# Performance work log

Hardware: AMD Instinct MI355X
Metric: run time of the kernel (lower is better)

The kernel has to match this reference:

```python
import jax, jax.numpy as jnp
import numpy as np

N = 1048576   # collocation points
D_IN = 2      # PDE spatial dim
H = 256       # mlp_x hidden
R0 = R1 = R2 = 64  # Tucker ranks (mlp_quad_last_shape)
NQ0 = NQ1 = 1024   # quadrature points per axis (quad_concat)
HQ = 128      # mlp_quad hidden
HC = 128      # core_mlp hidden
C_IN = 64     # core_init feature dim


def _mlp(x, W1, b1, W2, b2):
    # 2-layer MLP with tanh, standing in for the torch nn.Sequential MLPs
    return jnp.tanh(x @ W1 + b1) @ W2 + b2


def _r_func(quad_x, eq_param):
    # quadrature weight per point, shape (n_i, 1)
    return jnp.sin(jnp.pi * eq_param[0] * quad_x)


def setup_inputs() -> dict:
    key = jax.random.key(0)
    ks = jax.random.split(key, 16)

    def rn(k, shape, fan_in):
        return jax.random.normal(k, shape, dtype=jnp.float32) / np.float32(np.sqrt(fan_in))

    return {
        "input": jax.random.normal(ks[0], (N, D_IN), dtype=jnp.float32),
        "eq_param": jnp.ones((1,), jnp.float32),
        "quad_x0": jax.random.uniform(ks[1], (NQ0, 1), dtype=jnp.float32),
        "quad_x1": jax.random.uniform(ks[2], (NQ1, 1), dtype=jnp.float32),
        "core_init": jax.random.normal(ks[3], (1, C_IN), dtype=jnp.float32),
        # mlp_x: D_IN -> H -> R0
        "Wx1": rn(ks[4], (D_IN, H), D_IN), "bx1": jnp.zeros((H,), jnp.float32),
        "Wx2": rn(ks[5], (H, R0), H), "bx2": jnp.zeros((R0,), jnp.float32),
        # mlp_quad[0]: 1 -> HQ -> R1
        "Wq01": rn(ks[6], (1, HQ), 1), "bq01": jnp.zeros((HQ,), jnp.float32),
        "Wq02": rn(ks[7], (HQ, R1), HQ), "bq02": jnp.zeros((R1,), jnp.float32),
        # mlp_quad[1]: 1 -> HQ -> R2
        "Wq11": rn(ks[8], (1, HQ), 1), "bq11": jnp.zeros((HQ,), jnp.float32),
        "Wq12": rn(ks[9], (HQ, R2), HQ), "bq12": jnp.zeros((R2,), jnp.float32),
        # core_mlp: C_IN -> HC -> R0*R1*R2
        "Wc1": rn(ks[10], (C_IN, HC), C_IN), "bc1": jnp.zeros((HC,), jnp.float32),
        "Wc2": rn(ks[11], (HC, R0 * R1 * R2), HC), "bc2": jnp.zeros((R0 * R1 * R2,), jnp.float32),
    }


def reference(input, eq_param, quad_x0, quad_x1, core_init,
              Wx1, bx1, Wx2, bx2,
              Wq01, bq01, Wq02, bq02,
              Wq11, bq11, Wq12, bq12,
              Wc1, bc1, Wc2, bc2):
    # y, m = r_func(quad_x, eq_param) -> per-axis quadrature weights (n_i, 1)
    y0 = _r_func(quad_x0, eq_param)
    y1 = _r_func(quad_x1, eq_param)

    lhs = _mlp(input, Wx1, bx1, Wx2, bx2)                 # (N, R0)
    core = _mlp(core_init, Wc1, bc1, Wc2, bc2)            # (1, R0*R1*R2)
    core = core.reshape(R0, R1, R2)

    # loop axis 0: movedim(1,0) -> (R1,R0,R2), contract R1, sum quad points
    core = jnp.moveaxis(core, 1, 0)
    oq0 = y0 * _mlp(quad_x0, Wq01, bq01, Wq02, bq02)      # (NQ0, R1)
    # einsum('x...,cx->c...') then sum over c, fused:
    core = jnp.einsum('xab,cx->ab', core, oq0)            # (R0, R2)

    # loop axis 1: movedim(1,0) -> (R2,R0), contract R2, sum quad points
    core = jnp.moveaxis(core, 1, 0)
    oq1 = y1 * _mlp(quad_x1, Wq11, bq11, Wq12, bq12)      # (NQ1, R2)
    core = jnp.einsum('xa,cx->a', core, oq1)              # (R0,)

    # out = lhs @ core_out.T  (core_out is 1D -> vector output)
    return lhs @ core                                      # (N,)
```

## Files before the change

### kernel.cpp

```cpp
#include <hip/hip_runtime.h>
#include <hip/hip_bf16.h>
#include <stdint.h>

#define NPTS   1048576
#define HID    256
#define NQ     1024
#define HQ     128
#define HC     128
#define CIN    64
#define CORE_N 262144


#define TWO_LOG2E 2.885390081777927f

typedef float    v2f  __attribute__((ext_vector_type(2)));
typedef uint32_t u32x4 __attribute__((ext_vector_type(4)));
typedef float    f32x4 __attribute__((ext_vector_type(4)));

__device__ __forceinline__ bool sniff_bf16(const void* eq) {
    return ((const uint16_t*)eq)[0] == 0x3F80u;
}

__device__ __forceinline__ float ldv(const void* p, int i, bool b16) {
    return b16 ? __bfloat162float(((const __hip_bfloat16*)p)[i])
               : ((const float*)p)[i];
}

__device__ __forceinline__ float fast_tanh(float x) {
    float e = __builtin_amdgcn_exp2f(x * TWO_LOG2E);
    float r = __builtin_amdgcn_rcpf(e + 1.0f);
    return fmaf(-2.0f, r, 1.0f);
}

__global__ __launch_bounds__(1024) void k_small(
    const void* __restrict__ eq_param,
    const void* __restrict__ qx0, const void* __restrict__ qx1,
    const void* __restrict__ Wq01, const void* __restrict__ bq01,
    const void* __restrict__ Wq02, const void* __restrict__ bq02,
    const void* __restrict__ Wq11, const void* __restrict__ bq11,
    const void* __restrict__ Wq12, const void* __restrict__ bq12,
    const void* __restrict__ core_init,
    const void* __restrict__ Wc1, const void* __restrict__ bc1,
    float* __restrict__ ws)
{
    bool b16 = sniff_bf16(eq_param);
    int tid = threadIdx.x;
    int blk = blockIdx.x;
    if (blk == 2) {
        if (tid < HC) {
            float acc = ldv(bc1, tid, b16);
            for (int i = 0; i < CIN; ++i)
                acc = fmaf(ldv(core_init, i, b16), ldv(Wc1, i * HC + tid, b16), acc);
            ws[128 + tid] = fast_tanh(acc);
        } else if (tid < HC + 64) {
            ws[256 + (tid - HC) * 32] = 0.0f;
        }
        return;
    }
    const void* qx = blk ? qx1 : qx0;
    const void* W1 = blk ? Wq11 : Wq01;
    const void* b1 = blk ? bq11 : bq01;
    const void* W2 = blk ? Wq12 : Wq02;
    const void* b2 = blk ? bq12 : bq02;

    __shared__ float upart[8][HQ];
    __shared__ float ypart[8];
    __shared__ float uj[HQ];
    __shared__ float Ytot;

    int j = tid & 127;
    int cs = tid >> 7;
    float w1 = ldv(W1, j, b16), b1j = ldv(b1, j, b16);
    float eq = ldv(eq_param, 0, b16);
    const float PI = 3.14159265358979323846f;

    float u = 0.f, ysum = 0.f;
    for (int c = cs * 128; c < cs * 128 + 128; ++c) {
        float q = ldv(qx, c, b16);
        float y = __sinf(PI * eq * q);
        ysum += y;
        u += y * fast_tanh(fmaf(q, w1, b1j));
    }
    upart[cs][j] = u;
    if (j == 0) ypart[cs] = ysum;
    __syncthreads();
    if (tid < HQ) {
        float s = 0.f;
        for (int k = 0; k < 8; ++k) s += upart[k][tid];
        uj[tid] = s;
        if (tid == 0) { float Y = 0.f; for (int k = 0; k < 8; ++k) Y += ypart[k]; Ytot = Y; }
    }
    __syncthreads();
    if (tid < 64) {
        float s = Ytot * ldv(b2, tid, b16);
        for (int jj = 0; jj < HQ; ++jj) s = fmaf(uj[jj], ldv(W2, jj * 64 + tid, b16), s);
        ws[blk * 64 + tid] = s;
    }
}

__device__ __forceinline__ float chunk_dot_bf16(
    const u32x4* __restrict__ rp, int lane,
    const float* __restrict__ s0v, const float* __restrict__ s1v)
{
    float acc = 0.f;
    #pragma unroll
    for (int kk = 0; kk < 8; ++kk) {
        u32x4 v = __builtin_nontemporal_load(rp + kk * 64 + lane);
        float inner = 0.f;
        #pragma unroll
        for (int q = 0; q < 4; ++q) {
            float lo = __uint_as_float(v[q] << 16);
            float hi = __uint_as_float(v[q] & 0xffff0000u);
            inner = fmaf(lo, s1v[2 * q], inner);
            inner = fmaf(hi, s1v[2 * q + 1], inner);
        }
        acc = fmaf(inner, s0v[kk], acc);
    }
    return acc;
}

__device__ __forceinline__ float chunk_dot_f32(
    const f32x4* __restrict__ rp, int lane,
    const float* __restrict__ s0v, const float* __restrict__ s1v)
{
    float acc = 0.f;
    #pragma unroll
    for (int kk = 0; kk < 16; ++kk) {
        f32x4 v = __builtin_nontemporal_load(rp + kk * 64 + lane);
        float inner = v[0] * s1v[0];
        inner = fmaf(v[1], s1v[1], inner);
        inner = fmaf(v[2], s1v[2], inner);
        inner = fmaf(v[3], s1v[3], inner);
        acc = fmaf(inner, s0v[kk], acc);
    }
    return acc;
}

__global__ __launch_bounds__(256) void k_core(
    const void* __restrict__ Wc2, const void* __restrict__ bc2,
    const void* __restrict__ eq_param,
    const float* __restrict__ ws, float* __restrict__ cacc)
{
    bool b16 = sniff_bf16(eq_param);
    int tid = threadIdx.x;
    int lane = tid & 63;
    int W = blockIdx.x * 4 + (tid >> 6);
    int a = W & 63;
    int j0 = W >> 6;

    float acc = 0.f;
    if (b16) {
        int g = lane >> 3, yb = (lane & 7) * 8;
        float s1v[8], s0v[8];
        #pragma unroll
        for (int e = 0; e < 8; ++e) s1v[e] = ws[64 + yb + e];
        #pragma unroll
        for (int kk = 0; kk < 8; ++kk) s0v[kk] = ws[kk * 8 + g];

        const u32x4* base = (const u32x4*)((const __hip_bfloat16*)Wc2 + (size_t)a * 4096);
        const size_t rowstep = CORE_N / 8;
        #pragma unroll
        for (int k = 0; k < 2; ++k) {
            int j = j0 + 64 * k;
            float d = chunk_dot_bf16(base + (size_t)j * rowstep, lane, s0v, s1v);
            acc = fmaf(d, ws[128 + j], acc);
        }
        if (W < 64)
            acc += chunk_dot_bf16((const u32x4*)((const __hip_bfloat16*)bc2 + (size_t)a * 4096),
                                  lane, s0v, s1v);
    } else {
        int g = lane >> 4, yb = (lane & 15) * 4;
        float s1v[4], s0v[16];
        #pragma unroll
        for (int e = 0; e < 4; ++e) s1v[e] = ws[64 + yb + e];
        #pragma unroll
        for (int kk = 0; kk < 16; ++kk) s0v[kk] = ws[kk * 4 + g];

        const f32x4* base = (const f32x4*)((const float*)Wc2 + (size_t)a * 4096);
        const size_t rowstep = CORE_N / 4;
        #pragma unroll
        for (int k = 0; k < 2; ++k) {
            int j = j0 + 64 * k;
            float d = chunk_dot_f32(base + (size_t)j * rowstep, lane, s0v, s1v);
            acc = fmaf(d, ws[128 + j], acc);
        }
        if (W < 64)
            acc += chunk_dot_f32((const f32x4*)((const float*)bc2 + (size_t)a * 4096),
                                 lane, s0v, s1v);
    }

    for (int offl = 32; offl > 0; offl >>= 1) acc += __shfl_down(acc, offl);
    if (lane == 0) atomicAdd(&cacc[a * 32], acc);
}

__global__ __launch_bounds__(256) void k_prep(
    const void* __restrict__ Wx1, const void* __restrict__ bx1,
    const void* __restrict__ Wx2, const void* __restrict__ bx2,
    const void* __restrict__ eq_param,
    const float* __restrict__ cacc, float* __restrict__ ws)
{
    bool b16 = sniff_bf16(eq_param);
    __shared__ float cv[64];
    __shared__ float red[4];
    int tid = threadIdx.x;
    if (tid < 64) cv[tid] = cacc[tid * 32];
    __syncthreads();
    float w = 0.f;
    for (int a = 0; a < 64; ++a) w = fmaf(ldv(Wx2, tid * 64 + a, b16), cv[a], w);
    float4 t;
    t.x = TWO_LOG2E * ldv(Wx1, tid, b16);
    t.y = TWO_LOG2E * ldv(Wx1, HID + tid, b16);
    t.z = TWO_LOG2E * ldv(bx1, tid, b16);
    t.w = -2.0f * w;
    ((float4*)(ws + 2560))[tid] = t;

    float p = w + ((tid < 64) ? ldv(bx2, tid, b16) * cv[tid] : 0.f);
    for (int offl = 32; offl > 0; offl >>= 1) p += __shfl_down(p, offl);
    if ((tid & 63) == 0) red[tid >> 6] = p;
    __syncthreads();
    if (tid == 0) ws[3584] = red[0] + red[1] + red[2] + red[3];
}

__global__ __launch_bounds__(256) void k_main(
    const void* __restrict__ x, const void* __restrict__ eq_param,
    const float* __restrict__ ws, void* __restrict__ out)
{
    bool b16 = sniff_bf16(eq_param);
    const float4* __restrict__ tbl = (const float4*)(ws + 2560);
    const int stride = NPTS / 4;
    int p0 = blockIdx.x * 256 + threadIdx.x;

    float x0[4], x1[4];
    if (b16) {
        #pragma unroll
        for (int i = 0; i < 4; ++i) {
            uint32_t u = ((const uint32_t*)x)[p0 + i * stride];
            x0[i] = __uint_as_float(u << 16);
            x1[i] = __uint_as_float(u & 0xffff0000u);
        }
    } else {
        #pragma unroll
        for (int i = 0; i < 4; ++i) {
            float2 v = ((const float2*)x)[p0 + i * stride];
            x0[i] = v.x;
            x1[i] = v.y;
        }
    }
    v2f x0a = {x0[0], x0[1]}, x0b = {x0[2], x0[3]};
    v2f x1a = {x1[0], x1[1]}, x1b = {x1[2], x1[3]};

    float boff = ws[3584];
    v2f acca = {boff, boff}, accb = {boff, boff};

    #pragma unroll 4
    for (int jj = 0; jj < HID; ++jj) {
        float4 t = tbl[jj];
        v2f txv = {t.x, t.x}, tyv = {t.y, t.y}, tzv = {t.z, t.z}, twv = {t.w, t.w};
        v2f ga = x0a * txv + x1a * tyv + tzv;
        v2f gb = x0b * txv + x1b * tyv + tzv;
        ga.x = __builtin_fminf(ga.x, 30.0f); ga.y = __builtin_fminf(ga.y, 30.0f);
        gb.x = __builtin_fminf(gb.x, 30.0f); gb.y = __builtin_fminf(gb.y, 30.0f);
        v2f ea, eb;
        ea.x = __builtin_amdgcn_exp2f(ga.x); ea.y = __builtin_amdgcn_exp2f(ga.y);
        eb.x = __builtin_amdgcn_exp2f(gb.x); eb.y = __builtin_amdgcn_exp2f(gb.y);
        v2f onev = {1.0f, 1.0f};
        v2f Aa = ea + onev;
        v2f Ab = eb + onev;
        v2f R = Aa * Ab;
        float T = R.x * R.y;
        float tr = __builtin_amdgcn_rcpf(T);
        v2f rA;
        rA.x = R.y * tr;
        rA.y = R.x * tr;
        acca = twv * (Ab * rA) + acca;
        accb = twv * (Aa * rA) + accb;
    }
    float acc[4] = {acca.x, acca.y, accb.x, accb.y};
    if (b16) {
        #pragma unroll
        for (int i = 0; i < 4; ++i)
            ((__hip_bfloat16*)out)[p0 + i * stride] = __float2bfloat16(acc[i]);
    } else {
        #pragma unroll
        for (int i = 0; i < 4; ++i)
            ((float*)out)[p0 + i * stride] = acc[i];
    }
}

extern "C" void kernel_launch(void* const* d_in, const int* in_sizes, int n_in,
                              void* d_out, int out_size, void* d_ws, size_t ws_size,
                              hipStream_t stream) {
    (void)in_sizes; (void)n_in; (void)out_size; (void)ws_size;
    const void* input     = d_in[0];
    const void* eq_param  = d_in[1];
    const void* quad_x0   = d_in[2];
    const void* quad_x1   = d_in[3];
    const void* core_init = d_in[4];
    const void* Wx1  = d_in[5];
    const void* bx1  = d_in[6];
    const void* Wx2  = d_in[7];
    const void* bx2  = d_in[8];
    const void* Wq01 = d_in[9];
    const void* bq01 = d_in[10];
    const void* Wq02 = d_in[11];
    const void* bq02 = d_in[12];
    const void* Wq11 = d_in[13];
    const void* bq11 = d_in[14];
    const void* Wq12 = d_in[15];
    const void* bq12 = d_in[16];
    const void* Wc1  = d_in[17];
    const void* bc1  = d_in[18];
    const void* Wc2  = d_in[19];
    const void* bc2  = d_in[20];

    float* ws = (float*)d_ws;

    k_small<<<3, 1024, 0, stream>>>(eq_param, quad_x0, quad_x1,
                                    Wq01, bq01, Wq02, bq02,
                                    Wq11, bq11, Wq12, bq12,
                                    core_init, Wc1, bc1, ws);
    k_core<<<1024, 256, 0, stream>>>(Wc2, bc2, eq_param, ws, ws + 256);
    k_prep<<<1, 256, 0, stream>>>(Wx1, bx1, Wx2, bx2, eq_param, ws + 256, ws);
    k_main<<<NPTS / 1024, 256, 0, stream>>>(input, eq_param, ws, d_out);
}
```

Baseline: 340.0 us.

## Split quad MLP across blocks, fold small MLPs into core and prep into main

The quadrature kernel now runs on 8 blocks instead of 2, each emitting partial hidden sums. The second-layer quad projection and the core_init MLP are recomputed redundantly in every k_core block rather than in a serial prologue block. The k_prep kernel is removed: every k_main block rebuilds the 256-entry tanh table and bias offset in shared memory, with a vectorized Wx2 row dot. This cuts two launches and the serial tail latency, at the cost of redundant per-block work in k_core and k_main.

```diff
diff --git a/kernel.cpp b/kernel.cpp
--- a/kernel.cpp
+++ b/kernel.cpp
@@ -32,50 +32,34 @@
     return fmaf(-2.0f, r, 1.0f);
 }
 
-__global__ __launch_bounds__(1024) void k_small(
+__global__ __launch_bounds__(1024) void k_quad(
     const void* __restrict__ eq_param,
     const void* __restrict__ qx0, const void* __restrict__ qx1,
     const void* __restrict__ Wq01, const void* __restrict__ bq01,
-    const void* __restrict__ Wq02, const void* __restrict__ bq02,
     const void* __restrict__ Wq11, const void* __restrict__ bq11,
-    const void* __restrict__ Wq12, const void* __restrict__ bq12,
-    const void* __restrict__ core_init,
-    const void* __restrict__ Wc1, const void* __restrict__ bc1,
     float* __restrict__ ws)
 {
     bool b16 = sniff_bf16(eq_param);
     int tid = threadIdx.x;
-    int blk = blockIdx.x;
-    if (blk == 2) {
-        if (tid < HC) {
-            float acc = ldv(bc1, tid, b16);
-            for (int i = 0; i < CIN; ++i)
-                acc = fmaf(ldv(core_init, i, b16), ldv(Wc1, i * HC + tid, b16), acc);
-            ws[128 + tid] = fast_tanh(acc);
-        } else if (tid < HC + 64) {
-            ws[256 + (tid - HC) * 32] = 0.0f;
-        }
-        return;
-    }
-    const void* qx = blk ? qx1 : qx0;
-    const void* W1 = blk ? Wq11 : Wq01;
-    const void* b1 = blk ? bq11 : bq01;
-    const void* W2 = blk ? Wq12 : Wq02;
-    const void* b2 = blk ? bq12 : bq02;
-
-    __shared__ float upart[8][HQ];
+    int b = blockIdx.x;
+    int axis = b >> 2, bb = b & 3;
+    const void* qx = axis ? qx1 : qx0;
+    const void* W1 = axis ? Wq11 : Wq01;
+    const void* b1 = axis ? bq11 : bq01;
+
+    if (b == 0 && tid < 64) ws[1088 + tid * 32] = 0.0f;
+
+    __shared__ float upart[8][128];
     __shared__ float ypart[8];
-    __shared__ float uj[HQ];
-    __shared__ float Ytot;
-
-    int j = tid & 127;
-    int cs = tid >> 7;
+
+    int j = tid & 127, cs = tid >> 7;
     float w1 = ldv(W1, j, b16), b1j = ldv(b1, j, b16);
     float eq = ldv(eq_param, 0, b16);
     const float PI = 3.14159265358979323846f;
+    int c0 = bb * 256 + cs * 32;
 
     float u = 0.f, ysum = 0.f;
-    for (int c = cs * 128; c < cs * 128 + 128; ++c) {
+    for (int c = c0; c < c0 + 32; ++c) {
         float q = ldv(qx, c, b16);
         float y = __sinf(PI * eq * q);
         ysum += y;
@@ -84,17 +68,17 @@
     upart[cs][j] = u;
     if (j == 0) ypart[cs] = ysum;
     __syncthreads();
-    if (tid < HQ) {
+    if (tid < 128) {
         float s = 0.f;
+        #pragma unroll
         for (int k = 0; k < 8; ++k) s += upart[k][tid];
-        uj[tid] = s;
-        if (tid == 0) { float Y = 0.f; for (int k = 0; k < 8; ++k) Y += ypart[k]; Ytot = Y; }
-    }
-    __syncthreads();
-    if (tid < 64) {
-        float s = Ytot * ldv(b2, tid, b16);
-        for (int jj = 0; jj < HQ; ++jj) s = fmaf(uj[jj], ldv(W2, jj * 64 + tid, b16), s);
-        ws[blk * 64 + tid] = s;
+        ws[b * 128 + tid] = s;
+    }
+    if (tid == 0) {
+        float Y = 0.f;
+        #pragma unroll
+        for (int k = 0; k < 8; ++k) Y += ypart[k];
+        ws[1024 + b] = Y;
     }
 }
 
@@ -138,11 +122,48 @@
 
 __global__ __launch_bounds__(256) void k_core(
     const void* __restrict__ Wc2, const void* __restrict__ bc2,
+    const void* __restrict__ Wq02, const void* __restrict__ bq02,
+    const void* __restrict__ Wq12, const void* __restrict__ bq12,
+    const void* __restrict__ core_init,
+    const void* __restrict__ Wc1, const void* __restrict__ bc1,
     const void* __restrict__ eq_param,
     const float* __restrict__ ws, float* __restrict__ cacc)
 {
     bool b16 = sniff_bf16(eq_param);
     int tid = threadIdx.x;
+
+    __shared__ float u_l[256];
+    __shared__ float st[256];
+
+    {
+        int j = tid & 127, base = (tid >> 7) * 512;
+        float s = 0.f;
+        #pragma unroll
+        for (int k = 0; k < 4; ++k) s += ws[base + k * 128 + j];
+        u_l[tid] = s;
+    }
+    __syncthreads();
+    if (tid < 128) {
+        int a = tid & 63;
+        int axis = tid >> 6;
+        const void* W2 = axis ? Wq12 : Wq02;
+        const void* b2 = axis ? bq12 : bq02;
+        int yb = 1024 + axis * 4;
+        float Y = ws[yb] + ws[yb + 1] + ws[yb + 2] + ws[yb + 3];
+        float acc = Y * ldv(b2, a, b16);
+        const float* u = u_l + axis * 128;
+        for (int jj = 0; jj < HQ; ++jj)
+            acc = fmaf(u[jj], ldv(W2, jj * 64 + a, b16), acc);
+        st[tid] = acc;
+    } else {
+        int j = tid - 128;
+        float acc = ldv(bc1, j, b16);
+        for (int i = 0; i < CIN; ++i)
+            acc = fmaf(ldv(core_init, i, b16), ldv(Wc1, i * HC + j, b16), acc);
+        st[tid] = fast_tanh(acc);
+    }
+    __syncthreads();
+
     int lane = tid & 63;
     int W = blockIdx.x * 4 + (tid >> 6);
     int a = W & 63;
@@ -153,9 +174,9 @@
         int g = lane >> 3, yb = (lane & 7) * 8;
         float s1v[8], s0v[8];
         #pragma unroll
-        for (int e = 0; e < 8; ++e) s1v[e] = ws[64 + yb + e];
-        #pragma unroll
-        for (int kk = 0; kk < 8; ++kk) s0v[kk] = ws[kk * 8 + g];
+        for (int e = 0; e < 8; ++e) s1v[e] = st[64 + yb + e];
+        #pragma unroll
+        for (int kk = 0; kk < 8; ++kk) s0v[kk] = st[kk * 8 + g];
 
         const u32x4* base = (const u32x4*)((const __hip_bfloat16*)Wc2 + (size_t)a * 4096);
         const size_t rowstep = CORE_N / 8;
@@ -163,7 +184,7 @@
         for (int k = 0; k < 2; ++k) {
             int j = j0 + 64 * k;
             float d = chunk_dot_bf16(base + (size_t)j * rowstep, lane, s0v, s1v);
-            acc = fmaf(d, ws[128 + j], acc);
+            acc = fmaf(d, st[128 + j], acc);
         }
         if (W < 64)
             acc += chunk_dot_bf16((const u32x4*)((const __hip_bfloat16*)bc2 + (size_t)a * 4096),
@@ -172,9 +193,9 @@
         int g = lane >> 4, yb = (lane & 15) * 4;
         float s1v[4], s0v[16];
         #pragma unroll
-        for (int e = 0; e < 4; ++e) s1v[e] = ws[64 + yb + e];
-        #pragma unroll
-        for (int kk = 0; kk < 16; ++kk) s0v[kk] = ws[kk * 4 + g];
+        for (int e = 0; e < 4; ++e) s1v[e] = st[64 + yb + e];
+        #pragma unroll
+        for (int kk = 0; kk < 16; ++kk) s0v[kk] = st[kk * 4 + g];
 
         const f32x4* base = (const f32x4*)((const float*)Wc2 + (size_t)a * 4096);
         const size_t rowstep = CORE_N / 4;
@@ -182,7 +203,7 @@
         for (int k = 0; k < 2; ++k) {
             int j = j0 + 64 * k;
             float d = chunk_dot_f32(base + (size_t)j * rowstep, lane, s0v, s1v);
-            acc = fmaf(d, ws[128 + j], acc);
+            acc = fmaf(d, st[128 + j], acc);
         }
         if (W < 64)
             acc += chunk_dot_f32((const f32x4*)((const float*)bc2 + (size_t)a * 4096),
@@ -193,42 +214,59 @@
     if (lane == 0) atomicAdd(&cacc[a * 32], acc);
 }
 
-__global__ __launch_bounds__(256) void k_prep(
+__global__ __launch_bounds__(256) void k_main(
+    const void* __restrict__ x, const void* __restrict__ eq_param,
     const void* __restrict__ Wx1, const void* __restrict__ bx1,
     const void* __restrict__ Wx2, const void* __restrict__ bx2,
-    const void* __restrict__ eq_param,
-    const float* __restrict__ cacc, float* __restrict__ ws)
+    const float* __restrict__ cacc, void* __restrict__ out)
 {
     bool b16 = sniff_bf16(eq_param);
+    int tid = threadIdx.x;
     __shared__ float cv[64];
+    __shared__ float4 tbl[256];
     __shared__ float red[4];
-    int tid = threadIdx.x;
+
     if (tid < 64) cv[tid] = cacc[tid * 32];
     __syncthreads();
+
     float w = 0.f;
-    for (int a = 0; a < 64; ++a) w = fmaf(ldv(Wx2, tid * 64 + a, b16), cv[a], w);
-    float4 t;
-    t.x = TWO_LOG2E * ldv(Wx1, tid, b16);
-    t.y = TWO_LOG2E * ldv(Wx1, HID + tid, b16);
-    t.z = TWO_LOG2E * ldv(bx1, tid, b16);
-    t.w = -2.0f * w;
-    ((float4*)(ws + 2560))[tid] = t;
+    if (b16) {
+        const u32x4* wrow = (const u32x4*)((const __hip_bfloat16*)Wx2 + (size_t)tid * 64);
+        #pragma unroll
+        for (int q = 0; q < 8; ++q) {
+            u32x4 v = wrow[q];
+            #pragma unroll
+            for (int e = 0; e < 4; ++e) {
+                float lo = __uint_as_float(v[e] << 16);
+                float hi = __uint_as_float(v[e] & 0xffff0000u);
+                w = fmaf(lo, cv[q * 8 + 2 * e], w);
+                w = fmaf(hi, cv[q * 8 + 2 * e + 1], w);
+            }
+        }
+    } else {
+        const f32x4* wrow = (const f32x4*)((const float*)Wx2 + (size_t)tid * 64);
+        #pragma unroll
+        for (int q = 0; q < 16; ++q) {
+            f32x4 v = wrow[q];
+            #pragma unroll
+            for (int e = 0; e < 4; ++e) w = fmaf(v[e], cv[q * 4 + e], w);
+        }
+    }
+    float4 te;
+    te.x = TWO_LOG2E * ldv(Wx1, tid, b16);
+    te.y = TWO_LOG2E * ldv(Wx1, HID + tid, b16);
+    te.z = TWO_LOG2E * ldv(bx1, tid, b16);
+    te.w = -2.0f * w;
+    tbl[tid] = te;
 
     float p = w + ((tid < 64) ? ldv(bx2, tid, b16) * cv[tid] : 0.f);
     for (int offl = 32; offl > 0; offl >>= 1) p += __shfl_down(p, offl);
     if ((tid & 63) == 0) red[tid >> 6] = p;
     __syncthreads();
-    if (tid == 0) ws[3584] = red[0] + red[1] + red[2] + red[3];
-}
-
-__global__ __launch_bounds__(256) void k_main(
-    const void* __restrict__ x, const void* __restrict__ eq_param,
-    const float* __restrict__ ws, void* __restrict__ out)
-{
-    bool b16 = sniff_bf16(eq_param);
-    const float4* __restrict__ tbl = (const float4*)(ws + 2560);
+    float boff = red[0] + red[1] + red[2] + red[3];
+
     const int stride = NPTS / 4;
-    int p0 = blockIdx.x * 256 + threadIdx.x;
+    int p0 = blockIdx.x * 256 + tid;
 
     float x0[4], x1[4];
     if (b16) {
@@ -248,8 +286,6 @@
     }
     v2f x0a = {x0[0], x0[1]}, x0b = {x0[2], x0[3]};
     v2f x1a = {x1[0], x1[1]}, x1b = {x1[2], x1[3]};
-
-    float boff = ws[3584];
     v2f acca = {boff, boff}, accb = {boff, boff};
 
     #pragma unroll 4
@@ -315,11 +351,12 @@
 
     float* ws = (float*)d_ws;
 
-    k_small<<<3, 1024, 0, stream>>>(eq_param, quad_x0, quad_x1,
-                                    Wq01, bq01, Wq02, bq02,
-                                    Wq11, bq11, Wq12, bq12,
-                                    core_init, Wc1, bc1, ws);
-    k_core<<<1024, 256, 0, stream>>>(Wc2, bc2, eq_param, ws, ws + 256);
-    k_prep<<<1, 256, 0, stream>>>(Wx1, bx1, Wx2, bx2, eq_param, ws + 256, ws);
-    k_main<<<NPTS / 1024, 256, 0, stream>>>(input, eq_param, ws, d_out);
-}
+    k_quad<<<8, 1024, 0, stream>>>(eq_param, quad_x0, quad_x1,
+                                   Wq01, bq01, Wq11, bq11, ws);
+    k_core<<<1024, 256, 0, stream>>>(Wc2, bc2, Wq02, bq02, Wq12, bq12,
+                                     core_init, Wc1, bc1, eq_param,
+                                     ws, ws + 1088);
+    k_main<<<NPTS / 1024, 256, 0, stream>>>(input, eq_param,
+                                            Wx1, bx1, Wx2, bx2,
+                                            ws + 1088, d_out);
+}
```

Result: faster. 317.2 us (-6.7%).
